# Optimization experiments

Hardware: AMD Instinct MI355X
Metric: run time of the kernel (lower is better)

## Reference

```python
import jax, jax.numpy as jnp
from jax import lax
import numpy as np

B, L, C, H, F = 8, 512, 512, 8, 2048
NC, NA, K, W, S = 4, 6, 5, 4, 50
HD = C // H
R = 2 * W + 1
PAD = (K - 1) // 2
H2 = 2
HD2 = C // H2
VOCAB = 256
EPS = 1e-6


def ln_ch(x, g, b):
    # LayerNorm over channel dim of (B,C,L) (torch transposes to (B,L,C), norms last dim)
    m = jnp.mean(x, axis=1, keepdims=True)
    v = jnp.mean((x - m) ** 2, axis=1, keepdims=True)
    return (x - m) * lax.rsqrt(v + EPS) * g[None, :, None] + b[None, :, None]


def conv1x1(w, b, x):
    # 1x1 Conv1d == channel-mixing matmul
    return jnp.einsum('oc,bcl->bol', w, x) + b[None, :, None]


def forward_fn(tokens, style_values, mask, embed,
               cw_dw_w, cw_dw_b, cw_ln_g, cw_ln_b, cw_pw1_w, cw_pw1_b,
               cw_pw2_w, cw_pw2_b, cw_gamma,
               aq_w, aq_b, ak_w, ak_b, av_w, av_b, ao_w, ao_b,
               rel_k_emb, rel_v_emb, ln1_g, ln1_b, ln2_g, ln2_b,
               ffn_w1, ffn_b1, ffn_w2, ffn_b2,
               style_key, sq_w, sq_b, sk_w, sk_b, sv_w, sv_b, so_w, so_b,
               sn_g, sn_b):
    x = embed[tokens]                 # (B,L,C)
    x = jnp.transpose(x, (0, 2, 1))   # (B,C,L)

    # --- ConvNeXt stack ---
    for i in range(NC):
        x = x * mask
        res = x
        xp = jnp.pad(x, ((0, 0), (0, 0), (PAD, PAD)), mode='edge')  # replicate pad
        h = lax.conv_general_dilated(xp, cw_dw_w[i][:, None, :], (1,), 'VALID',
                                     feature_group_count=C,
                                     dimension_numbers=('NCH', 'OIH', 'NCH'))
        h = h + cw_dw_b[i][None, :, None]
        h = h * mask
        h = ln_ch(h, cw_ln_g[i], cw_ln_b[i])
        h = conv1x1(cw_pw1_w[i], cw_pw1_b[i], h)
        h = jax.nn.gelu(h, approximate=False)
        h = conv1x1(cw_pw2_w[i], cw_pw2_b[i], h)
        x = res + cw_gamma[i][None, :, None] * h
        x = x * mask

    # --- AttnEncoder with windowed relative-position attention ---
    x = x * mask
    attn_mask = mask[:, :, :, None] * mask[:, :, None, :]   # (B,1,L,L)
    t = jnp.arange(L)
    diff = t[None, :] - t[:, None]
    wmask = (jnp.abs(diff) <= W).astype(x.dtype)             # (L,L)
    idx = jnp.clip(diff, -W, W) + W                          # (L,L) in [0,2W]
    scale = HD ** -0.5
    for i in range(NA):
        res = x
        q = conv1x1(aq_w[i], aq_b[i], x).reshape(B, H, HD, L).transpose(0, 1, 3, 2) * scale
        k = conv1x1(ak_w[i], ak_b[i], x).reshape(B, H, HD, L).transpose(0, 1, 3, 2)
        v = conv1x1(av_w[i], av_b[i], x).reshape(B, H, HD, L).transpose(0, 1, 3, 2)
        scores = jnp.einsum('bhld,bhmd->bhlm', q, k)
        rel_k = rel_k_emb[i][idx]                             # (L,L,HD)
        scores = scores + jnp.einsum('bhld,lmd->bhlm', q, rel_k) * wmask[None, None]
        scores = jnp.where(attn_mask == 0, -10000.0, scores)
        attn = jax.nn.softmax(scores, axis=-1)
        out = jnp.einsum('bhlm,bhmd->bhld', attn, v)
        rel_v = rel_v_emb[i][idx] * wmask[:, :, None]         # (L,L,HD)
        out = out + jnp.einsum('bhlm,lmd->bhld', attn, rel_v)
        out = out.transpose(0, 1, 3, 2).reshape(B, C, L)
        out = conv1x1(ao_w[i], ao_b[i], out)
        x = ln_ch(res + out, ln1_g[i], ln1_b[i])
        h = conv1x1(ffn_w1[i], ffn_b1[i], x * mask)
        h = jax.nn.relu(h) * mask
        h = conv1x1(ffn_w2[i], ffn_b2[i], h) * mask
        x = ln_ch(x + h, ln2_g[i], ln2_b[i])
    x = x * mask

    # --- StyleAttention ---
    xt = jnp.transpose(x, (0, 2, 1))          # (B,L,C)
    mask_t = jnp.transpose(mask, (0, 2, 1))   # (B,L,1)
    sscale = C ** -0.5                         # torch uses full dim, not head_dim

    def style_layer(xin, i):
        q = (xin @ sq_w[i].T + sq_b[i]).reshape(B, L, H2, HD2)
        kk = jnp.tanh(style_key[0] @ sk_w[i].T + sk_b[i]).reshape(S, H2, HD2)
        vals = jnp.broadcast_to(style_values, (B, S, C))
        vv = (vals @ sv_w[i].T + sv_b[i]).reshape(B, S, H2, HD2)
        sc = jnp.einsum('bthd,shd->hbts', q, kk) * sscale
        a = jax.nn.softmax(sc, axis=-1)
        a = jnp.where(mask_t[None] == 0, 0.0, a)
        o = jnp.einsum('hbts,bshd->bthd', a, vv).reshape(B, L, C)
        o = o @ so_w[i].T + so_b[i]
        return o * mask_t

    out1 = style_layer(xt, 0)
    x1 = xt + out1
    out2 = style_layer(x1, 1)
    x2 = xt + out2
    m = jnp.mean(x2, axis=-1, keepdims=True)
    var = jnp.mean((x2 - m) ** 2, axis=-1, keepdims=True)
    xn = (x2 - m) * lax.rsqrt(var + EPS) * sn_g + sn_b
    x = jnp.transpose(xn, (0, 2, 1)) * mask
    return x


def setup_inputs() -> dict:
    key = jax.random.key(0)
    kit = iter(jax.random.split(key, 48))

    def rn(shape, s=0.02):
        return jax.random.normal(next(kit), shape, jnp.float32) * s

    inp = {
        'tokens': jax.random.randint(next(kit), (B, L), 0, VOCAB),
        'style_values': rn((1, S, C), 1.0),
        'mask': jnp.ones((B, 1, L), jnp.float32),
        'embed': rn((VOCAB, C), 1.0),
        'cw_dw_w': rn((NC, C, K)), 'cw_dw_b': jnp.zeros((NC, C)),
        'cw_ln_g': jnp.ones((NC, C)), 'cw_ln_b': jnp.zeros((NC, C)),
        'cw_pw1_w': rn((NC, 4 * C, C)), 'cw_pw1_b': jnp.zeros((NC, 4 * C)),
        'cw_pw2_w': rn((NC, C, 4 * C)), 'cw_pw2_b': jnp.zeros((NC, C)),
        'cw_gamma': jnp.full((NC, C), 1e-6, jnp.float32),
        'aq_w': rn((NA, C, C)), 'aq_b': jnp.zeros((NA, C)),
        'ak_w': rn((NA, C, C)), 'ak_b': jnp.zeros((NA, C)),
        'av_w': rn((NA, C, C)), 'av_b': jnp.zeros((NA, C)),
        'ao_w': rn((NA, C, C)), 'ao_b': jnp.zeros((NA, C)),
        'rel_k_emb': rn((NA, R, HD)), 'rel_v_emb': rn((NA, R, HD)),
        'ln1_g': jnp.ones((NA, C)), 'ln1_b': jnp.zeros((NA, C)),
        'ln2_g': jnp.ones((NA, C)), 'ln2_b': jnp.zeros((NA, C)),
        'ffn_w1': rn((NA, F, C)), 'ffn_b1': jnp.zeros((NA, F)),
        'ffn_w2': rn((NA, C, F)), 'ffn_b2': jnp.zeros((NA, C)),
        'style_key': rn((1, S, C)),
        'sq_w': rn((2, C, C)), 'sq_b': jnp.zeros((2, C)),
        'sk_w': rn((2, C, C)), 'sk_b': jnp.zeros((2, C)),
        'sv_w': rn((2, C, C)), 'sv_b': jnp.zeros((2, C)),
        'so_w': rn((2, C, C)), 'so_b': jnp.zeros((2, C)),
        'sn_g': jnp.ones((C,)), 'sn_b': jnp.zeros((C,)),
    }
    return inp


def reference(tokens, style_values, mask, embed,
              cw_dw_w, cw_dw_b, cw_ln_g, cw_ln_b, cw_pw1_w, cw_pw1_b,
              cw_pw2_w, cw_pw2_b, cw_gamma,
              aq_w, aq_b, ak_w, ak_b, av_w, av_b, ao_w, ao_b,
              rel_k_emb, rel_v_emb, ln1_g, ln1_b, ln2_g, ln2_b,
              ffn_w1, ffn_b1, ffn_w2, ffn_b2,
              style_key, sq_w, sq_b, sk_w, sk_b, sv_w, sv_b, so_w, so_b,
              sn_g, sn_b):
    return forward_fn(tokens, style_values, mask, embed,
                      cw_dw_w, cw_dw_b, cw_ln_g, cw_ln_b, cw_pw1_w, cw_pw1_b,
                      cw_pw2_w, cw_pw2_b, cw_gamma,
                      aq_w, aq_b, ak_w, ak_b, av_w, av_b, ao_w, ao_b,
                      rel_k_emb, rel_v_emb, ln1_g, ln1_b, ln2_g, ln2_b,
                      ffn_w1, ffn_b1, ffn_w2, ffn_b2,
                      style_key, sq_w, sq_b, sk_w, sk_b, sv_w, sv_b, so_w, so_b,
                      sn_g, sn_b)
```

## Files before the change

kernel.cpp:

```cpp
#include <hip/hip_runtime.h>
#include <cstdint>

#define Bb 8
#define Ll 512
#define Cc 512
#define Hh 8
#define HD 64
#define Ff 2048
#define Ss 50
#define NROWS 4096
#define QKVS 1536

typedef __attribute__((ext_vector_type(8))) short short8v;
typedef __attribute__((ext_vector_type(4))) float f32x4;

__device__ __forceinline__ float wave_sum(float v){
  #pragma unroll
  for (int o=32;o>=1;o>>=1) v += __shfl_xor(v,o);
  return v;
}
__device__ __forceinline__ float wave_max(float v){
  #pragma unroll
  for (int o=32;o>=1;o>>=1) v = fmaxf(v,__shfl_xor(v,o));
  return v;
}
__device__ __forceinline__ float bf2f(unsigned short u){
  return __uint_as_float(((unsigned)u) << 16);
}

__device__ __forceinline__ void splitc(float a, unsigned short& hi, unsigned short& lo){
  unsigned u = __float_as_uint(a);
  hi = (unsigned short)(u >> 16);
  float l = a - __uint_as_float(u & 0xFFFF0000u);
  lo = (unsigned short)(__float_as_uint(l) >> 16);
}
__device__ __forceinline__ void split4(float4 v, unsigned short* hi, unsigned short* lo){
  unsigned short h0,h1,h2,h3,l0,l1,l2,l3;
  splitc(v.x,h0,l0); splitc(v.y,h1,l1); splitc(v.z,h2,l2); splitc(v.w,h3,l3);
  *(ushort4*)hi = make_ushort4(h0,h1,h2,h3);
  *(ushort4*)lo = make_ushort4(l0,l1,l2,l3);
}

__global__ __launch_bounds__(256) void split_all(
    const float* __restrict__ pw1w, const float* __restrict__ pw2w,
    const float* __restrict__ aow,  const float* __restrict__ f1w,
    const float* __restrict__ f2w,  const float* __restrict__ sqw,
    const float* __restrict__ sow,
    const float* __restrict__ aqw, const float* __restrict__ akw,
    const float* __restrict__ avw,
    unsigned short* __restrict__ pw1h, unsigned short* __restrict__ pw1l,
    unsigned short* __restrict__ pw2h, unsigned short* __restrict__ pw2l,
    unsigned short* __restrict__ aoh,  unsigned short* __restrict__ aol,
    unsigned short* __restrict__ f1h,  unsigned short* __restrict__ f1l,
    unsigned short* __restrict__ f2h,  unsigned short* __restrict__ f2l,
    unsigned short* __restrict__ sqh,  unsigned short* __restrict__ sql,
    unsigned short* __restrict__ soh,  unsigned short* __restrict__ sol,
    unsigned short* __restrict__ qkvh, unsigned short* __restrict__ qkvl)
{
  int seg = blockIdx.y;
  if (seg == 7){
    const int n4 = 6*QKVS*512/4;
    for (int i = blockIdx.x*256 + threadIdx.x; i < n4; i += gridDim.x*256){
      int e = i << 2;
      int layer = e / 786432;
      int r = e - layer*786432;
      int which = r >> 18;
      int off = r & 262143;
      const float* s = (which==0) ? aqw : (which==1) ? akw : avw;
      float4 vv = *(const float4*)(s + (size_t)layer*262144 + off);
      split4(vv, (unsigned short*)((ushort4*)qkvh + i),
                 (unsigned short*)((ushort4*)qkvl + i));
    }
    return;
  }
  const float* src; unsigned short* hi; unsigned short* lo; int n4;
  switch(seg){
    case 0: src=pw1w; hi=pw1h; lo=pw1l; n4=1048576; break;
    case 1: src=pw2w; hi=pw2h; lo=pw2l; n4=1048576; break;
    case 2: src=aow;  hi=aoh;  lo=aol;  n4=393216;  break;
    case 3: src=f1w;  hi=f1h;  lo=f1l;  n4=1572864; break;
    case 4: src=f2w;  hi=f2h;  lo=f2l;  n4=1572864; break;
    case 5: src=sqw;  hi=sqh;  lo=sql;  n4=131072;  break;
    default: src=sow; hi=soh;  lo=sol;  n4=131072;  break;
  }
  for (int i = blockIdx.x*256 + threadIdx.x; i < n4; i += gridDim.x*256){
    float4 v = ((const float4*)src)[i];
    split4(v, (unsigned short*)((ushort4*)hi + i), (unsigned short*)((ushort4*)lo + i));
  }
}

__global__ __launch_bounds__(128) void embed_k(const int* __restrict__ tok,
    const float* __restrict__ emb, const float* __restrict__ mask,
    float* __restrict__ x){
  int n = blockIdx.x;
  int t = tok[n];
  float m = mask[n];
  float4 v = ((const float4*)(emb + ((size_t)t<<9)))[threadIdx.x];
  v.x*=m; v.y*=m; v.z*=m; v.w*=m;
  ((float4*)(x + ((size_t)n<<9)))[threadIdx.x] = v;
}

__global__ __launch_bounds__(128) void dwln_k(const float* __restrict__ x,
    const float* __restrict__ w, const float* __restrict__ bias,
    const float* __restrict__ mask, const float* __restrict__ g,
    const float* __restrict__ bt, unsigned short* __restrict__ yh,
    unsigned short* __restrict__ yl){
  __shared__ float ws1[2], ws2[2];
  int n = blockIdx.x; int b_ = n >> 9, l = n & 511;
  int c0 = threadIdx.x * 4;
  float a0=bias[c0], a1=bias[c0+1], a2=bias[c0+2], a3=bias[c0+3];
  #pragma unroll
  for (int k=0;k<5;k++){
    int ls = l + k - 2; ls = ls < 0 ? 0 : (ls > 511 ? 511 : ls);
    const float4 xv = *(const float4*)&x[((size_t)(b_*512 + ls) << 9) + c0];
    a0 += w[(c0+0)*5+k]*xv.x;
    a1 += w[(c0+1)*5+k]*xv.y;
    a2 += w[(c0+2)*5+k]*xv.z;
    a3 += w[(c0+3)*5+k]*xv.w;
  }
  float mm = mask[n];
  a0*=mm; a1*=mm; a2*=mm; a3*=mm;
  int wv = threadIdx.x >> 6, ln_ = threadIdx.x & 63;
  float s = wave_sum(a0+a1+a2+a3);
  if (ln_ == 0) ws1[wv] = s;
  __syncthreads();
  float mean = (ws1[0] + ws1[1]) * (1.f/512.f);
  float d0=a0-mean, d1=a1-mean, d2=a2-mean, d3=a3-mean;
  float sq = wave_sum(d0*d0+d1*d1+d2*d2+d3*d3);
  if (ln_ == 0) ws2[wv] = sq;
  __syncthreads();
  float var = (ws2[0] + ws2[1]) * (1.f/512.f);
  float inv = 1.f/sqrtf(var + 1e-6f);
  float4 gv = *(const float4*)&g[c0];
  float4 bv = *(const float4*)&bt[c0];
  float4 o;
  o.x = d0*inv*gv.x + bv.x;
  o.y = d1*inv*gv.y + bv.y;
  o.z = d2*inv*gv.z + bv.z;
  o.w = d3*inv*gv.w + bv.w;
  size_t base = ((size_t)n << 9) + c0;
  split4(o, yh+base, yl+base);
}

template<bool SPLIT, bool MASK>
__global__ __launch_bounds__(256) void ln_rows(const float* __restrict__ x,
    const float* __restrict__ g, const float* __restrict__ bt,
    const float* __restrict__ rowmask,
    float* __restrict__ y, unsigned short* __restrict__ yh,
    unsigned short* __restrict__ yl, int nrows){
  int wid = threadIdx.x >> 6, lane = threadIdx.x & 63;
  int row = blockIdx.x*4 + wid;
  if (row >= nrows) return;
  const float4* xr = (const float4*)(x + ((size_t)row<<9));
  float4 a = xr[lane*2], b = xr[lane*2+1];
  float s = a.x+a.y+a.z+a.w+b.x+b.y+b.z+b.w;
  s = wave_sum(s);
  float m = s * (1.f/512.f);
  float d0=a.x-m,d1=a.y-m,d2=a.z-m,d3=a.w-m,d4=b.x-m,d5=b.y-m,d6=b.z-m,d7=b.w-m;
  float sq = d0*d0+d1*d1+d2*d2+d3*d3+d4*d4+d5*d5+d6*d6+d7*d7;
  sq = wave_sum(sq);
  float var = sq * (1.f/512.f);
  float inv = 1.f/sqrtf(var + 1e-6f);
  const float4* gr = (const float4*)g; const float4* br = (const float4*)bt;
  float4 g0=gr[lane*2], g1=gr[lane*2+1], b0=br[lane*2], b1=br[lane*2+1];
  float4 o0, o1;
  o0.x=d0*inv*g0.x+b0.x; o0.y=d1*inv*g0.y+b0.y; o0.z=d2*inv*g0.z+b0.z; o0.w=d3*inv*g0.w+b0.w;
  o1.x=d4*inv*g1.x+b1.x; o1.y=d5*inv*g1.y+b1.y; o1.z=d6*inv*g1.z+b1.z; o1.w=d7*inv*g1.w+b1.w;
  if constexpr (MASK){
    float mf = rowmask[row];
    o0.x*=mf; o0.y*=mf; o0.z*=mf; o0.w*=mf;
    o1.x*=mf; o1.y*=mf; o1.z*=mf; o1.w*=mf;
  }
  float4* yr = (float4*)(y + ((size_t)row<<9));
  yr[lane*2]=o0; yr[lane*2+1]=o1;
  if constexpr (SPLIT){
    size_t base = ((size_t)row<<9) + lane*8;
    split4(o0, yh+base,   yl+base);
    split4(o1, yh+base+4, yl+base+4);
  }
}

#define EPI_BIAS 0
#define EPI_SCALE 1
#define EPI_GELU 2
#define EPI_RES 3
#define EPI_RELU_MASK 4
#define EPI_RES_MASK 5
#define EPI_RES_GAMMA_MASK 6
#define EPI_TANH 7
#define EPI_QKV 8

__global__ __launch_bounds__(256) void style_prep(
    const float* __restrict__ style_key, const float* __restrict__ style_v,
    const float* __restrict__ sk_w, const float* __restrict__ sk_b,
    const float* __restrict__ sv_w, const float* __restrict__ sv_b,
    float* __restrict__ KK, float* __restrict__ VV)
{
  __shared__ float As[16][68];
  __shared__ float Bs[16][68];
  int sel = blockIdx.y;
  const float* A = (sel < 2) ? style_key : style_v;
  const float* W = (sel==0) ? sk_w : (sel==1) ? sk_w+262144 :
                   (sel==2) ? sv_w : sv_w+262144;
  const float* bias = (sel==0) ? sk_b : (sel==1) ? sk_b+512 :
                      (sel==2) ? sv_b : sv_b+512;
  float* Y = (sel==0) ? KK : (sel==1) ? KK+25600 :
             (sel==2) ? VV : VV+25600;
  bool do_tanh = (sel < 2);
  const int N = 50, K = 512, O = 512;
  int t = threadIdx.x;
  int tx = t & 15, ty = t >> 4;
  int col0 = blockIdx.x << 6;
  int lr = t >> 2, lk = (t & 3) << 2;
  float acc[4][4] = {};
  int ar = lr;
  bool arok = ar < N;
  const float* Ap = A + (size_t)(arok ? ar : 0) * K + lk;
  const float* Wp = W + (size_t)(col0 + lr) * K + lk;
  for (int k0 = 0; k0 < K; k0 += 16) {
    float4 av;
    if (arok) av = *(const float4*)(Ap + k0);
    else { av.x=0;av.y=0;av.z=0;av.w=0; }
    float4 bv = *(const float4*)(Wp + k0);
    As[lk+0][lr]=av.x; As[lk+1][lr]=av.y; As[lk+2][lr]=av.z; As[lk+3][lr]=av.w;
    Bs[lk+0][lr]=bv.x; Bs[lk+1][lr]=bv.y; Bs[lk+2][lr]=bv.z; Bs[lk+3][lr]=bv.w;
    __syncthreads();
    #pragma unroll
    for (int k=0;k<16;k++){
      float4 af = *(const float4*)&As[k][ty<<2];
      float4 bf = *(const float4*)&Bs[k][tx<<2];
      float a4[4]={af.x,af.y,af.z,af.w};
      float b4[4]={bf.x,bf.y,bf.z,bf.w};
      #pragma unroll
      for (int i=0;i<4;i++)
        #pragma unroll
        for (int j=0;j<4;j++)
          acc[i][j] += a4[i]*b4[j];
    }
    __syncthreads();
  }
  #pragma unroll
  for (int i=0;i<4;i++){
    int row = (ty<<2) + i;
    if (row >= N) break;
    int colb = col0 + (tx<<2);
    float vv_[4];
    #pragma unroll
    for (int j=0;j<4;j++){
      float v = acc[i][j] + bias[colb+j];
      if (do_tanh) v = tanhf(v);
      vv_[j]=v;
    }
    float4 ov; ov.x=vv_[0]; ov.y=vv_[1]; ov.z=vv_[2]; ov.w=vv_[3];
    *(float4*)(Y + (size_t)row*O + colb) = ov;
  }
}

template<int EPI, bool AMASK, int OUT, int NF>
__global__ __launch_bounds__(256) void gemm_ps(
    const unsigned short* __restrict__ Ah, const unsigned short* __restrict__ Al,
    const unsigned short* __restrict__ Wh, const unsigned short* __restrict__ Wl,
    const float* __restrict__ bias, const float* __restrict__ res,
    const float* __restrict__ gamma, const float* __restrict__ rowmask,
    float* __restrict__ Y, unsigned short* __restrict__ Yh,
    unsigned short* __restrict__ Yl, unsigned short* __restrict__ VTh,
    unsigned short* __restrict__ VTl, int K, int O, float scale)
{
  __shared__ unsigned short AhS[2][64][40], AlS[2][64][40];
  __shared__ unsigned short BhS[2][NF*32][40], BlS[2][NF*32][40];
  int t = threadIdx.x;
  int row0 = blockIdx.y << 6;
  int col0 = blockIdx.x << (NF==4 ? 7 : 6);
  int lane = t & 63, wid = t >> 6;
  int wr = wid >> 1, wc = wid & 1;

  int sr = t >> 2, sc = (t & 3) << 3;
  const unsigned short* Ahg = Ah + (size_t)(row0 + sr)*K + sc;
  const unsigned short* Alg = Al + (size_t)(row0 + sr)*K + sc;
  const unsigned short* Bhg = Wh + (size_t)(col0 + sr)*K + sc;
  const unsigned short* Blg = Wl + (size_t)(col0 + sr)*K + sc;
  float am = 1.f;
  if (AMASK) am = rowmask[row0 + sr];

  f32x4 acc[2][NF] = {};
  int nsteps = K >> 5;
  short8v ah_, al_, bh0_, bl0_, bh1_, bl1_;
  ah_ = *(const short8v*)(Ahg);
  al_ = *(const short8v*)(Alg);
  bh0_ = *(const short8v*)(Bhg);
  bl0_ = *(const short8v*)(Blg);
  if constexpr (NF==4){
    bh1_ = *(const short8v*)(Bhg + (size_t)64*K);
    bl1_ = *(const short8v*)(Blg + (size_t)64*K);
  }
  if (AMASK && am == 0.f){ ah_ ^= ah_; al_ ^= al_; }
  *(short8v*)&AhS[0][sr][sc] = ah_;
  *(short8v*)&AlS[0][sr][sc] = al_;
  *(short8v*)&BhS[0][sr][sc] = bh0_;
  *(short8v*)&BlS[0][sr][sc] = bl0_;
  if constexpr (NF==4){
    *(short8v*)&BhS[0][sr+64][sc] = bh1_;
    *(short8v*)&BlS[0][sr+64][sc] = bl1_;
  }

  int st = 0;
  for (int s = 0; s < nsteps; ++s){
    if (s+1 < nsteps){
      int ko = (s+1) << 5;
      ah_ = *(const short8v*)(Ahg + ko);
      al_ = *(const short8v*)(Alg + ko);
      bh0_ = *(const short8v*)(Bhg + ko);
      bl0_ = *(const short8v*)(Blg + ko);
      if constexpr (NF==4){
        bh1_ = *(const short8v*)(Bhg + (size_t)64*K + ko);
        bl1_ = *(const short8v*)(Blg + (size_t)64*K + ko);
      }
      if (AMASK && am == 0.f){ ah_ ^= ah_; al_ ^= al_; }
    }
    __syncthreads();
    int fr = lane & 15, fc = (lane >> 4) << 3;
    short8v ahf[2], alf[2], bhf[NF], blf[NF];
    #pragma unroll
    for (int mt=0; mt<2; ++mt){
      int r = (wr<<5) + (mt<<4) + fr;
      ahf[mt] = *(const short8v*)&AhS[st][r][fc];
      alf[mt] = *(const short8v*)&AlS[st][r][fc];
    }
    #pragma unroll
    for (int nt=0; nt<NF; ++nt){
      int r = (NF==4 ? (wc<<6) : (wc<<5)) + (nt<<4) + fr;
      bhf[nt] = *(const short8v*)&BhS[st][r][fc];
      blf[nt] = *(const short8v*)&BlS[st][r][fc];
    }
    #pragma unroll
    for (int mt=0; mt<2; ++mt)
      #pragma unroll
      for (int nt=0; nt<NF; ++nt){
        f32x4 c = acc[mt][nt];
        c = __builtin_amdgcn_mfma_f32_16x16x32_bf16(ahf[mt], bhf[nt], c, 0,0,0);
        c = __builtin_amdgcn_mfma_f32_16x16x32_bf16(ahf[mt], blf[nt], c, 0,0,0);
        c = __builtin_amdgcn_mfma_f32_16x16x32_bf16(alf[mt], bhf[nt], c, 0,0,0);
        acc[mt][nt] = c;
      }
    if (s+1 < nsteps){
      int nb = st ^ 1;
      *(short8v*)&AhS[nb][sr][sc] = ah_;
      *(short8v*)&AlS[nb][sr][sc] = al_;
      *(short8v*)&BhS[nb][sr][sc] = bh0_;
      *(short8v*)&BlS[nb][sr][sc] = bl0_;
      if constexpr (NF==4){
        *(short8v*)&BhS[nb][sr+64][sc] = bh1_;
        *(short8v*)&BlS[nb][sr+64][sc] = bl1_;
      }
    }
    st ^= 1;
  }

  int rb = row0 + (wr<<5) + ((lane>>4)<<2);
  int cb = col0 + (NF==4 ? (wc<<6) : (wc<<5)) + (lane & 15);
  float bs[NF], gm[NF];
  int which = 0;
  if constexpr (EPI==EPI_QKV) which = blockIdx.x >> 2;
  #pragma unroll
  for (int nt=0; nt<NF; ++nt){
    int col = cb + (nt<<4);
    if constexpr (EPI==EPI_QKV){
      const float* bp = (which==0) ? bias : (which==1) ? res : gamma;
      bs[nt] = bp[col & 511];
    } else {
      bs[nt] = bias[col];
      if constexpr (EPI==EPI_RES_GAMMA_MASK) gm[nt] = gamma[col];
    }
  }
  float qscale = 1.f;
  if constexpr (EPI==EPI_QKV) qscale = (which==0) ? scale : 1.f;

  if constexpr (OUT==2){
    if (which == 2){
      #pragma unroll
      for (int mt=0; mt<2; ++mt){
        int row = rb + (mt<<4);
        int b = row >> 9, tok = row & 511;
        #pragma unroll
        for (int nt=0; nt<NF; ++nt){
          int dglob = cb + (nt<<4) - 1024;
          size_t vt = ((size_t)b*512 + dglob)*512 + tok;
          unsigned short h4[4], l4[4];
          #pragma unroll
          for (int j=0; j<4; ++j)
            splitc(acc[mt][nt][j] + bs[nt], h4[j], l4[j]);
          *(ushort4*)&VTh[vt] = make_ushort4(h4[0],h4[1],h4[2],h4[3]);
          *(ushort4*)&VTl[vt] = make_ushort4(l4[0],l4[1],l4[2],l4[3]);
        }
      }
      return;
    }
    #pragma unroll
    for (int mt=0; mt<2; ++mt)
      #pragma unroll
      for (int j=0; j<4; ++j){
        int row = rb + (mt<<4) + j;
        #pragma unroll
        for (int nt=0; nt<NF; ++nt){
          float v = (acc[mt][nt][j] + bs[nt]) * qscale;
          size_t oidx = (size_t)row*O + cb + (nt<<4);
          unsigned short h,l; splitc(v,h,l); Yh[oidx]=h; Yl[oidx]=l;
        }
      }
// ... 241 lines not shown
  short8v ah0 = *(const short8v*)&Qh[fr][fc];
  short8v ah1 = *(const short8v*)&Qh[fr][32+fc];
  short8v al0 = *(const short8v*)&Ql[fr][fc];
  short8v al1 = *(const short8v*)&Ql[fr][32+fc];

  if (w == 0){
    short8v rh0 = *(const short8v*)&Rkh[fr][fc];
    short8v rh1 = *(const short8v*)&Rkh[fr][32+fc];
    short8v rl0 = *(const short8v*)&Rkl[fr][fc];
    short8v rl1 = *(const short8v*)&Rkl[fr][32+fc];
    f32x4 c4 = {};
    c4 = __builtin_amdgcn_mfma_f32_16x16x32_bf16(ah0,rh0,c4,0,0,0);
    c4 = __builtin_amdgcn_mfma_f32_16x16x32_bf16(ah1,rh1,c4,0,0,0);
    c4 = __builtin_amdgcn_mfma_f32_16x16x32_bf16(ah0,rl0,c4,0,0,0);
    c4 = __builtin_amdgcn_mfma_f32_16x16x32_bf16(ah1,rl1,c4,0,0,0);
    c4 = __builtin_amdgcn_mfma_f32_16x16x32_bf16(al0,rh0,c4,0,0,0);
    c4 = __builtin_amdgcn_mfma_f32_16x16x32_bf16(al1,rh1,c4,0,0,0);
    #pragma unroll
    for (int j = 0; j < 4; ++j) qrel[qbase + j][fr] = c4[j];
  }
  __syncthreads();

  f32x4 sreg[8];
  #pragma unroll
  for (int tt = 0; tt < 8; ++tt){
    int br = tt*64 + w*16 + fr;
    const unsigned short* krh = Ph_g + (rowoff + br)*QKVS + 512 + h*64;
    const unsigned short* krl = Pl_g + (rowoff + br)*QKVS + 512 + h*64;
    short8v bh0 = *(const short8v*)(krh + fc);
    short8v bh1 = *(const short8v*)(krh + 32 + fc);
    short8v bl0 = *(const short8v*)(krl + fc);
    short8v bl1 = *(const short8v*)(krl + 32 + fc);
    f32x4 c4 = {};
    c4 = __builtin_amdgcn_mfma_f32_16x16x32_bf16(ah0,bh0,c4,0,0,0);
    c4 = __builtin_amdgcn_mfma_f32_16x16x32_bf16(ah1,bh1,c4,0,0,0);
    c4 = __builtin_amdgcn_mfma_f32_16x16x32_bf16(ah0,bl0,c4,0,0,0);
    c4 = __builtin_amdgcn_mfma_f32_16x16x32_bf16(ah1,bl1,c4,0,0,0);
    c4 = __builtin_amdgcn_mfma_f32_16x16x32_bf16(al0,bh0,c4,0,0,0);
    c4 = __builtin_amdgcn_mfma_f32_16x16x32_bf16(al1,bh1,c4,0,0,0);
    int m = tt*64 + w*16 + fr;
    float mm_ = ms_[m];
    #pragma unroll
    for (int j = 0; j < 4; ++j){
      int q = qbase + j;
      int l = l0 + q;
      float s = c4[j];
      int dlt = m - l + 4;
      if (dlt >= 0 && dlt <= 8) s += qrel[q][dlt];
      if (ms_[l] * mm_ == 0.f) s = -10000.f;
      c4[j] = s;
    }
    sreg[tt] = c4;
  }

  float mx[4], sm[4], inv[4];
  #pragma unroll
  for (int j = 0; j < 4; ++j){
    float v = sreg[0][j];
    #pragma unroll
    for (int tt = 1; tt < 8; ++tt) v = fmaxf(v, sreg[tt][j]);
    #pragma unroll
    for (int o = 8; o >= 1; o >>= 1) v = fmaxf(v, __shfl_xor(v, o));
    mx[j] = v;
  }
  if (fr == 0){
    #pragma unroll
    for (int j = 0; j < 4; ++j) red1[w][qbase + j] = mx[j];
  }
  __syncthreads();
  #pragma unroll
  for (int j = 0; j < 4; ++j){
    int q = qbase + j;
    mx[j] = fmaxf(fmaxf(red1[0][q], red1[1][q]), fmaxf(red1[2][q], red1[3][q]));
  }
  #pragma unroll
  for (int j = 0; j < 4; ++j) sm[j] = 0.f;
  #pragma unroll
  for (int tt = 0; tt < 8; ++tt){
    f32x4 c4 = sreg[tt];
    #pragma unroll
    for (int j = 0; j < 4; ++j){
      float e = expf(c4[j] - mx[j]);
      c4[j] = e;
      sm[j] += e;
    }
    sreg[tt] = c4;
  }
  #pragma unroll
  for (int j = 0; j < 4; ++j){
    float v = sm[j];
    #pragma unroll
    for (int o = 8; o >= 1; o >>= 1) v += __shfl_xor(v, o);
    sm[j] = v;
  }
  if (fr == 0){
    #pragma unroll
    for (int j = 0; j < 4; ++j) red2[w][qbase + j] = sm[j];
  }
  #pragma unroll
  for (int tt = 0; tt < 8; ++tt){
    int m = tt*64 + w*16 + fr;
    #pragma unroll
    for (int j = 0; j < 4; ++j){
      unsigned short hh, ll_;
      splitc(sreg[tt][j], hh, ll_);
      Sh[qbase + j][m] = hh; Sl[qbase + j][m] = ll_;
    }
  }
  __syncthreads();
  #pragma unroll
  for (int j = 0; j < 4; ++j){
    int q = qbase + j;
    inv[j] = 1.f / (red2[0][q] + red2[1][q] + red2[2][q] + red2[3][q]);
  }

  f32x4 oacc = {};
  const unsigned short* vrh = VTh_g + ((size_t)b_*512 + h*64 + w*16 + fr)*512;
  const unsigned short* vrl = VTl_g + ((size_t)b_*512 + h*64 + w*16 + fr)*512;
  #pragma unroll
  for (int tt = 0; tt < 8; ++tt){
    #pragma unroll
    for (int ks = 0; ks < 2; ++ks){
      int moff = tt*64 + ks*32 + fc;
      short8v ah = *(const short8v*)&Sh[fr][moff];
      short8v al = *(const short8v*)&Sl[fr][moff];
      short8v bh = *(const short8v*)(vrh + moff);
      short8v bl = *(const short8v*)(vrl + moff);
      oacc = __builtin_amdgcn_mfma_f32_16x16x32_bf16(ah,bh,oacc,0,0,0);
      oacc = __builtin_amdgcn_mfma_f32_16x16x32_bf16(ah,bl,oacc,0,0,0);
      oacc = __builtin_amdgcn_mfma_f32_16x16x32_bf16(al,bh,oacc,0,0,0);
    }
  }
  {
    int d = w*16 + fr;
    #pragma unroll
    for (int j = 0; j < 4; ++j){
      int q = qbase + j;
      int l = l0 + q;
      float val = oacc[j];
      #pragma unroll
      for (int dlt = 0; dlt < 9; ++dlt){
        int m = l + dlt - 4;
        if (m >= 0 && m < 512){
          float e = bf2f(Sh[q][m]) + bf2f(Sl[q][m]);
          val += e * rv[dlt][d];
        }
      }
      val *= inv[j];
      unsigned short hh, ll_; splitc(val, hh, ll_);
      size_t oidx = ((rowoff + l) << 9) + h*64 + d;
      Oh[oidx] = hh; Ol[oidx] = ll_;
    }
  }
}

__global__ __launch_bounds__(128) void style_attn_k(const float* __restrict__ Q,
    const float* __restrict__ kk, const float* __restrict__ vv,
    const float* __restrict__ mask, unsigned short* __restrict__ Oh,
    unsigned short* __restrict__ Ol){
  int n = blockIdx.x;
  int h = threadIdx.x >> 6, lane = threadIdx.x & 63;
  __shared__ float qh[512];
  __shared__ float aw[2][64];
  {
    float4 v = ((const float4*)(Q + ((size_t)n<<9)))[threadIdx.x];
    *(float4*)&qh[threadIdx.x*4] = v;
  }
  __syncthreads();
  float sc;
  if (lane < 50){
    float s = 0.f;
    const float* kr = kk + lane*512 + h*256;
    const float* qr = qh + h*256;
    for (int d4 = 0; d4 < 64; ++d4){
      float4 kv = *(const float4*)&kr[d4*4];
      s += qr[d4*4]*kv.x + qr[d4*4+1]*kv.y + qr[d4*4+2]*kv.z + qr[d4*4+3]*kv.w;
    }
    sc = s * 0.044194173824159216f;
  } else sc = -1e30f;
  float mx = wave_max(sc);
  float ex = (lane < 50) ? expf(sc - mx) : 0.f;
  float sm = wave_sum(ex);
  float keep = (mask[n] == 0.f) ? 0.f : 1.f;
  aw[h][lane] = ex / sm * keep;
  __syncthreads();
  float4 acc; acc.x=0; acc.y=0; acc.z=0; acc.w=0;
  const float* vb = vv + h*256 + lane*4;
  for (int s = 0; s < 50; ++s){
    float a = aw[h][s];
    const float4 vvv = *(const float4*)&vb[(size_t)s*512];
    acc.x += a*vvv.x; acc.y += a*vvv.y; acc.z += a*vvv.z; acc.w += a*vvv.w;
  }
  size_t oidx = ((size_t)n<<9) + h*256 + lane*4;
  split4(acc, Oh+oidx, Ol+oidx);
}

__global__ __launch_bounds__(256) void transpose_out_k(const float* __restrict__ xn,
    const float* __restrict__ mask, float* __restrict__ out){
  __shared__ float tile[32][33];
  int b_ = blockIdx.z; int c0 = blockIdx.x*32; int l0 = blockIdx.y*32;
  int tx = threadIdx.x & 31, ty = threadIdx.x >> 5;
  #pragma unroll
  for (int r=0;r<4;r++){
    int l = l0 + ty + r*8;
    tile[ty + r*8][tx] = xn[(((size_t)(b_*512 + l))<<9) + c0 + tx];
  }
  __syncthreads();
  float mm = mask[b_*512 + l0 + tx];
  #pragma unroll
  for (int r=0;r<4;r++){
    int c = c0 + ty + r*8;
    out[(((size_t)(b_*512 + c))<<9) + l0 + tx] = tile[tx][ty + r*8] * mm;
  }
}

extern "C" void kernel_launch(void* const* d_in, const int* in_sizes, int n_in,
                              void* d_out, int out_size, void* d_ws, size_t ws_size,
                              hipStream_t stream) {
  const int*   tokens   = (const int*)  d_in[0];
  const float* style_v  = (const float*)d_in[1];
  const float* mask     = (const float*)d_in[2];
  const float* embed_w  = (const float*)d_in[3];
  const float* cw_dw_w  = (const float*)d_in[4];
  const float* cw_dw_b  = (const float*)d_in[5];
  const float* cw_ln_g  = (const float*)d_in[6];
  const float* cw_ln_b  = (const float*)d_in[7];
  const float* cw_pw1_w = (const float*)d_in[8];
  const float* cw_pw1_b = (const float*)d_in[9];
  const float* cw_pw2_w = (const float*)d_in[10];
  const float* cw_pw2_b = (const float*)d_in[11];
  const float* cw_gamma = (const float*)d_in[12];
  const float* aq_w = (const float*)d_in[13];
  const float* aq_b = (const float*)d_in[14];
  const float* ak_w = (const float*)d_in[15];
  const float* ak_b = (const float*)d_in[16];
  const float* av_w = (const float*)d_in[17];
  const float* av_b = (const float*)d_in[18];
  const float* ao_w = (const float*)d_in[19];
  const float* ao_b = (const float*)d_in[20];
  const float* rel_k = (const float*)d_in[21];
  const float* rel_v = (const float*)d_in[22];
  const float* ln1_g = (const float*)d_in[23];
  const float* ln1_b = (const float*)d_in[24];
  const float* ln2_g = (const float*)d_in[25];
  const float* ln2_b = (const float*)d_in[26];
  const float* ffn_w1 = (const float*)d_in[27];
  const float* ffn_b1 = (const float*)d_in[28];
  const float* ffn_w2 = (const float*)d_in[29];
  const float* ffn_b2 = (const float*)d_in[30];
  const float* style_key = (const float*)d_in[31];
  const float* sq_w = (const float*)d_in[32];
  const float* sq_b = (const float*)d_in[33];
  const float* sk_w = (const float*)d_in[34];
  const float* sk_b = (const float*)d_in[35];
  const float* sv_w = (const float*)d_in[36];
  const float* sv_b = (const float*)d_in[37];
  const float* so_w = (const float*)d_in[38];
  const float* so_b = (const float*)d_in[39];
  const float* sn_g = (const float*)d_in[40];
  const float* sn_b = (const float*)d_in[41];

  const int N = NROWS;
  char* cur = (char*)d_ws;
  auto nextF = [&](size_t n)->float*{ float* p=(float*)cur; cur += n*sizeof(float); return p; };
  auto nextU = [&](size_t n)->unsigned short*{ unsigned short* p=(unsigned short*)cur; cur += n*2; return p; };

  float* X   = nextF((size_t)N*512);
  float* T   = nextF((size_t)N*512);
  float* Qb  = nextF((size_t)N*512);
  float* Vb  = nextF((size_t)N*512);
  float* KK  = nextF(2*50*512);
  float* VV  = nextF(2*50*512);
  unsigned short* Xh = nextU((size_t)N*512);
  unsigned short* Xl = nextU((size_t)N*512);
  unsigned short* Th = nextU((size_t)N*512);
  unsigned short* Tl = nextU((size_t)N*512);
  unsigned short* Hbh = nextU((size_t)N*2048);
  unsigned short* Hbl = nextU((size_t)N*2048);
  unsigned short* QKVh = nextU((size_t)N*QKVS);
  unsigned short* QKVl = nextU((size_t)N*QKVS);
  unsigned short* VTh = nextU((size_t)8*512*512);
  unsigned short* VTl = nextU((size_t)8*512*512);
  unsigned short* pw1h = nextU(4194304); unsigned short* pw1l = nextU(4194304);
  unsigned short* pw2h = nextU(4194304); unsigned short* pw2l = nextU(4194304);
  unsigned short* qkvh = nextU((size_t)6*QKVS*512); unsigned short* qkvl = nextU((size_t)6*QKVS*512);
  unsigned short* aoh  = nextU(1572864); unsigned short* aol  = nextU(1572864);
  unsigned short* f1h  = nextU(6291456); unsigned short* f1l  = nextU(6291456);
  unsigned short* f2h  = nextU(6291456); unsigned short* f2l  = nextU(6291456);
  unsigned short* sqh  = nextU(524288);  unsigned short* sql  = nextU(524288);
  unsigned short* soh  = nextU(524288);  unsigned short* sol  = nextU(524288);

  split_all<<<dim3(512,8),256,0,stream>>>(cw_pw1_w, cw_pw2_w, ao_w, ffn_w1,
      ffn_w2, sq_w, so_w, aq_w, ak_w, av_w,
      pw1h, pw1l, pw2h, pw2l, aoh, aol, f1h, f1l, f2h, f2l,
      sqh, sql, soh, sol, qkvh, qkvl);

  dim3 gm512(8,64), gbig2048(16,32), gbigqkv(12,32);

  embed_k<<<4096,128,0,stream>>>(tokens, embed_w, mask, X);

  for (int i=0;i<4;i++){
    dwln_k<<<4096,128,0,stream>>>(X, cw_dw_w + (size_t)i*512*5, cw_dw_b + i*512,
        mask, cw_ln_g+i*512, cw_ln_b+i*512, Th, Tl);
    gemm_big<EPI_GELU,false,1><<<gbig2048,256,0,stream>>>(Th, Tl,
        pw1h + (size_t)i*1048576, pw1l + (size_t)i*1048576,
        cw_pw1_b+i*2048, nullptr, nullptr, nullptr, nullptr, Hbh, Hbl,
        nullptr, nullptr, 512, 2048, 0.f);
    if (i < 3)
      gemm_ps<EPI_RES_GAMMA_MASK,false,0,2><<<gm512,256,0,stream>>>(Hbh, Hbl,
          pw2h + (size_t)i*1048576, pw2l + (size_t)i*1048576,
          cw_pw2_b+i*512, X, cw_gamma+i*512, mask, X, nullptr, nullptr,
          nullptr, nullptr, 2048, 512, 0.f);
    else
      gemm_ps<EPI_RES_GAMMA_MASK,false,3,2><<<gm512,256,0,stream>>>(Hbh, Hbl,
          pw2h + (size_t)i*1048576, pw2l + (size_t)i*1048576,
          cw_pw2_b+i*512, X, cw_gamma+i*512, mask, X, Xh, Xl,
          nullptr, nullptr, 2048, 512, 0.f);
  }

  for (int i=0;i<6;i++){
    gemm_big<EPI_QKV,false,2><<<gbigqkv,256,0,stream>>>(Xh, Xl,
        qkvh + (size_t)i*QKVS*512, qkvl + (size_t)i*QKVS*512,
        aq_b+i*512, ak_b+i*512, av_b+i*512, nullptr, nullptr, QKVh, QKVl,
        VTh, VTl, 512, QKVS, 0.125f);
    attn_mf<<<2048,256,0,stream>>>(QKVh, QKVl, VTh, VTl,
        rel_k + (size_t)i*9*64, rel_v + (size_t)i*9*64, mask, Th, Tl);
    gemm_ps<EPI_RES,false,0,2><<<gm512,256,0,stream>>>(Th, Tl,
        aoh + (size_t)i*262144, aol + (size_t)i*262144,
        ao_b+i*512, X, nullptr, nullptr, Qb, nullptr, nullptr,
        nullptr, nullptr, 512, 512, 0.f);
    ln_rows<true,false><<<1024,256,0,stream>>>(Qb, ln1_g+i*512, ln1_b+i*512,
        nullptr, X, Xh, Xl, N);
    gemm_big<EPI_RELU_MASK,true,1><<<gbig2048,256,0,stream>>>(Xh, Xl,
        f1h + (size_t)i*1048576, f1l + (size_t)i*1048576,
        ffn_b1+i*2048, nullptr, nullptr, mask, nullptr, Hbh, Hbl,
        nullptr, nullptr, 512, 2048, 0.f);
    gemm_ps<EPI_RES_MASK,false,0,2><<<gm512,256,0,stream>>>(Hbh, Hbl,
        f2h + (size_t)i*1048576, f2l + (size_t)i*1048576,
        ffn_b2+i*512, X, nullptr, mask, Qb, nullptr, nullptr,
        nullptr, nullptr, 2048, 512, 0.f);
    if (i < 5)
      ln_rows<true,false><<<1024,256,0,stream>>>(Qb, ln2_g+i*512, ln2_b+i*512,
          nullptr, X, Xh, Xl, N);
    else
      ln_rows<true,true><<<1024,256,0,stream>>>(Qb, ln2_g+i*512, ln2_b+i*512,
          mask, X, Xh, Xl, N);
  }

  style_prep<<<dim3(8,4),256,0,stream>>>(style_key, style_v, sk_w, sk_b,
      sv_w, sv_b, KK, VV);

  gemm_ps<EPI_BIAS,false,0,2><<<gm512,256,0,stream>>>(Xh, Xl, sqh, sql,
      sq_b, nullptr, nullptr, nullptr, Qb, nullptr, nullptr,
      nullptr, nullptr, 512, 512, 0.f);
  style_attn_k<<<4096,128,0,stream>>>(Qb, KK, VV, mask, Th, Tl);
  gemm_ps<EPI_RES_MASK,false,1,2><<<gm512,256,0,stream>>>(Th, Tl, soh, sol,
      so_b, X, nullptr, mask, nullptr, Hbh, Hbl,
      nullptr, nullptr, 512, 512, 0.f);
  gemm_ps<EPI_BIAS,false,0,2><<<gm512,256,0,stream>>>(Hbh, Hbl, sqh+262144, sql+262144,
      sq_b+512, nullptr, nullptr, nullptr, Qb, nullptr, nullptr,
      nullptr, nullptr, 512, 512, 0.f);
  style_attn_k<<<4096,128,0,stream>>>(Qb, KK+25600, VV+25600, mask, Th, Tl);
  gemm_ps<EPI_RES_MASK,false,0,2><<<gm512,256,0,stream>>>(Th, Tl, soh+262144, sol+262144,
      so_b+512, X, nullptr, mask, Vb, nullptr, nullptr,
      nullptr, nullptr, 512, 512, 0.f);

  ln_rows<false,false><<<1024,256,0,stream>>>(Vb, sn_g, sn_b, nullptr,
      Qb, nullptr, nullptr, N);
  transpose_out_k<<<dim3(16,16,8),256,0,stream>>>(Qb, mask, (float*)d_out);
}
```

Measured before the change: 1.890 ms.

## Run style attention on MFMA with split-bf16 Q, K and transposed V

Replaces the scalar FP32 style-attention kernel, which used one block per query row, with an MFMA kernel. Each block handles 16 rows for both heads and uses split hi/lo bf16 operands (three MFMAs per product) for Q·K and P·V. style_prep now writes K and a transposed V in split bf16 with padding to 64 keys, and the Q projection emits split bf16 instead of fp32. This moves the style attention onto the matrix units at the cost of serial softmax on 32 threads and a small loss in precision from the split-bf16 scheme.

```diff
diff --git a/kernel.cpp b/kernel.cpp
--- a/kernel.cpp
+++ b/kernel.cpp
@@ -17,11 +17,6 @@
 __device__ __forceinline__ float wave_sum(float v){
   #pragma unroll
   for (int o=32;o>=1;o>>=1) v += __shfl_xor(v,o);
-  return v;
-}
-__device__ __forceinline__ float wave_max(float v){
-  #pragma unroll
-  for (int o=32;o>=1;o>>=1) v = fmaxf(v,__shfl_xor(v,o));
   return v;
 }
 __device__ __forceinline__ float bf2f(unsigned short u){
@@ -194,28 +189,27 @@
     const float* __restrict__ style_key, const float* __restrict__ style_v,
     const float* __restrict__ sk_w, const float* __restrict__ sk_b,
     const float* __restrict__ sv_w, const float* __restrict__ sv_b,
-    float* __restrict__ KK, float* __restrict__ VV)
+    unsigned short* __restrict__ KKh, unsigned short* __restrict__ KKl,
+    unsigned short* __restrict__ VTh_s, unsigned short* __restrict__ VTl_s)
 {
   __shared__ float As[16][68];
   __shared__ float Bs[16][68];
   int sel = blockIdx.y;
-  const float* A = (sel < 2) ? style_key : style_v;
+  bool is_k = (sel < 2);
+  int layer = sel & 1;
+  const float* A = is_k ? style_key : style_v;
   const float* W = (sel==0) ? sk_w : (sel==1) ? sk_w+262144 :
                    (sel==2) ? sv_w : sv_w+262144;
   const float* bias = (sel==0) ? sk_b : (sel==1) ? sk_b+512 :
                       (sel==2) ? sv_b : sv_b+512;
-  float* Y = (sel==0) ? KK : (sel==1) ? KK+25600 :
-             (sel==2) ? VV : VV+25600;
-  bool do_tanh = (sel < 2);
-  const int N = 50, K = 512, O = 512;
+  const int N = 50, K = 512;
   int t = threadIdx.x;
   int tx = t & 15, ty = t >> 4;
   int col0 = blockIdx.x << 6;
   int lr = t >> 2, lk = (t & 3) << 2;
   float acc[4][4] = {};
-  int ar = lr;
-  bool arok = ar < N;
-  const float* Ap = A + (size_t)(arok ? ar : 0) * K + lk;
+  bool arok = lr < N;
+  const float* Ap = A + (size_t)(arok ? lr : 0) * K + lk;
   const float* Wp = W + (size_t)(col0 + lr) * K + lk;
   for (int k0 = 0; k0 < K; k0 += 16) {
     float4 av;
@@ -242,18 +236,114 @@
   #pragma unroll
   for (int i=0;i<4;i++){
     int row = (ty<<2) + i;
-    if (row >= N) break;
-    int colb = col0 + (tx<<2);
-    float vv_[4];
     #pragma unroll
     for (int j=0;j<4;j++){
-      float v = acc[i][j] + bias[colb+j];
-      if (do_tanh) v = tanhf(v);
-      vv_[j]=v;
-    }
-    float4 ov; ov.x=vv_[0]; ov.y=vv_[1]; ov.z=vv_[2]; ov.w=vv_[3];
-    *(float4*)(Y + (size_t)row*O + colb) = ov;
-  }
+      int col = col0 + (tx<<2) + j;
+      int head = col >> 8, d = col & 255;
+      float v = 0.f;
+      if (row < N){
+        v = acc[i][j] + bias[col];
+        if (is_k) v = tanhf(v);
+      }
+      unsigned short hh, ll_;
+      splitc(v, hh, ll_);
+      if (is_k){
+        size_t o = (((size_t)layer*2 + head)<<14) + row*256 + d;
+        KKh[o]=hh; KKl[o]=ll_;
+      } else {
+        size_t o = (((size_t)layer*2 + head)<<14) + d*64 + row;
+        VTh_s[o]=hh; VTl_s[o]=ll_;
+      }
+    }
+  }
+}
+
+__global__ __launch_bounds__(256) void style_mf(
+    const unsigned short* __restrict__ Qh_g, const unsigned short* __restrict__ Ql_g,
+    const unsigned short* __restrict__ KKh, const unsigned short* __restrict__ KKl,
+    const unsigned short* __restrict__ VTh_s, const unsigned short* __restrict__ VTl_s,
+    const float* __restrict__ mask,
+    unsigned short* __restrict__ Oh, unsigned short* __restrict__ Ol)
+{
+  __shared__ float Sc[2][16][68];
+  __shared__ unsigned short Pph[2][16][72], Ppl[2][16][72];
+  int t = threadIdx.x, lane = t & 63, w = t >> 6;
+  int head = w >> 1, nh = w & 1;
+  int rowbase = blockIdx.x * 16;
+  int fr = lane & 15, fc = (lane >> 4) << 3, qbase = (lane >> 4) << 2;
+
+  f32x4 s2[2] = {};
+  #pragma unroll
+  for (int ks = 0; ks < 8; ++ks){
+    size_t qoff = (size_t)(rowbase + fr)*512 + head*256 + ks*32 + fc;
+    short8v ah = *(const short8v*)(Qh_g + qoff);
+    short8v al = *(const short8v*)(Ql_g + qoff);
+    #pragma unroll
+    for (int nt = 0; nt < 2; ++nt){
+      int key = nh*32 + nt*16 + fr;
+      size_t ko = (((size_t)head)<<14) + key*256 + ks*32 + fc;
+      short8v bh = *(const short8v*)(KKh + ko);
+      short8v bl = *(const short8v*)(KKl + ko);
+      f32x4 c = s2[nt];
+      c = __builtin_amdgcn_mfma_f32_16x16x32_bf16(ah,bh,c,0,0,0);
+      c = __builtin_amdgcn_mfma_f32_16x16x32_bf16(ah,bl,c,0,0,0);
+      c = __builtin_amdgcn_mfma_f32_16x16x32_bf16(al,bh,c,0,0,0);
+      s2[nt] = c;
+    }
+  }
+  #pragma unroll
+  for (int nt = 0; nt < 2; ++nt)
+    #pragma unroll
+    for (int j = 0; j < 4; ++j)
+      Sc[head][qbase+j][nh*32 + nt*16 + fr] = s2[nt][j] * 0.044194173824159216f;
+  __syncthreads();
+
+  if (t < 32){
+    int h2 = t >> 4, r = t & 15;
+    float mx = -3.4e38f;
+    for (int ss = 0; ss < 50; ++ss) mx = fmaxf(mx, Sc[h2][r][ss]);
+    float sum = 0.f;
+    for (int ss = 0; ss < 50; ++ss) sum += expf(Sc[h2][r][ss] - mx);
+    float keep = (mask[rowbase + r] == 0.f) ? 0.f : 1.f;
+    float inv = keep / sum;
+    for (int ss = 0; ss < 64; ++ss){
+      float p = (ss < 50) ? expf(Sc[h2][r][ss] - mx) * inv : 0.f;
+      unsigned short hh, ll_;
+      splitc(p, hh, ll_);
+      Pph[h2][r][ss] = hh; Ppl[h2][r][ss] = ll_;
+    }
+  }
+  __syncthreads();
+
+  f32x4 av[8] = {};
+  #pragma unroll
+  for (int ks = 0; ks < 2; ++ks){
+    short8v ah = *(const short8v*)&Pph[head][fr][ks*32 + fc];
+    short8v al = *(const short8v*)&Ppl[head][fr][ks*32 + fc];
+    #pragma unroll
+    for (int nt = 0; nt < 8; ++nt){
+      int d = nh*128 + nt*16 + fr;
+      size_t vo = (((size_t)head)<<14) + d*64 + ks*32 + fc;
+      short8v bh = *(const short8v*)(VTh_s + vo);
+      short8v bl = *(const short8v*)(VTl_s + vo);
+      f32x4 c = av[nt];
+      c = __builtin_amdgcn_mfma_f32_16x16x32_bf16(ah,bh,c,0,0,0);
+      c = __builtin_amdgcn_mfma_f32_16x16x32_bf16(ah,bl,c,0,0,0);
+      c = __builtin_amdgcn_mfma_f32_16x16x32_bf16(al,bh,c,0,0,0);
+      av[nt] = c;
+    }
+  }
+  #pragma unroll
+  for (int nt = 0; nt < 8; ++nt)
+    #pragma unroll
+    for (int j = 0; j < 4; ++j){
+      int row = rowbase + qbase + j;
+      int d = nh*128 + nt*16 + fr;
+      unsigned short hh, ll_;
+      splitc(av[nt][j], hh, ll_);
+      size_t o = (size_t)row*512 + head*256 + d;
+      Oh[o] = hh; Ol[o] = ll_;
+    }
 }
 
 template<int EPI, bool AMASK, int OUT, int NF>
@@ -801,47 +891,6 @@
       Oh[oidx] = hh; Ol[oidx] = ll_;
     }
   }
-}
-
-__global__ __launch_bounds__(128) void style_attn_k(const float* __restrict__ Q,
-    const float* __restrict__ kk, const float* __restrict__ vv,
-    const float* __restrict__ mask, unsigned short* __restrict__ Oh,
-    unsigned short* __restrict__ Ol){
-  int n = blockIdx.x;
-  int h = threadIdx.x >> 6, lane = threadIdx.x & 63;
-  __shared__ float qh[512];
-  __shared__ float aw[2][64];
-  {
-    float4 v = ((const float4*)(Q + ((size_t)n<<9)))[threadIdx.x];
-    *(float4*)&qh[threadIdx.x*4] = v;
-  }
-  __syncthreads();
-  float sc;
-  if (lane < 50){
-    float s = 0.f;
-    const float* kr = kk + lane*512 + h*256;
-    const float* qr = qh + h*256;
-    for (int d4 = 0; d4 < 64; ++d4){
-      float4 kv = *(const float4*)&kr[d4*4];
-      s += qr[d4*4]*kv.x + qr[d4*4+1]*kv.y + qr[d4*4+2]*kv.z + qr[d4*4+3]*kv.w;
-    }
-    sc = s * 0.044194173824159216f;
-  } else sc = -1e30f;
-  float mx = wave_max(sc);
-  float ex = (lane < 50) ? expf(sc - mx) : 0.f;
-  float sm = wave_sum(ex);
-  float keep = (mask[n] == 0.f) ? 0.f : 1.f;
-  aw[h][lane] = ex / sm * keep;
-  __syncthreads();
-  float4 acc; acc.x=0; acc.y=0; acc.z=0; acc.w=0;
-  const float* vb = vv + h*256 + lane*4;
-  for (int s = 0; s < 50; ++s){
-    float a = aw[h][s];
-    const float4 vvv = *(const float4*)&vb[(size_t)s*512];
-    acc.x += a*vvv.x; acc.y += a*vvv.y; acc.z += a*vvv.z; acc.w += a*vvv.w;
-  }
-  size_t oidx = ((size_t)n<<9) + h*256 + lane*4;
-  split4(acc, Oh+oidx, Ol+oidx);
 }
 
 __global__ __launch_bounds__(256) void transpose_out_k(const float* __restrict__ xn,
@@ -918,8 +967,6 @@
   float* T   = nextF((size_t)N*512);
   float* Qb  = nextF((size_t)N*512);
   float* Vb  = nextF((size_t)N*512);
-  float* KK  = nextF(2*50*512);
-  float* VV  = nextF(2*50*512);
   unsigned short* Xh = nextU((size_t)N*512);
   unsigned short* Xl = nextU((size_t)N*512);
   unsigned short* Th = nextU((size_t)N*512);
@@ -938,6 +985,8 @@
   unsigned short* f2h  = nextU(6291456); unsigned short* f2l  = nextU(6291456);
   unsigned short* sqh  = nextU(524288);  unsigned short* sql  = nextU(524288);
   unsigned short* soh  = nextU(524288);  unsigned short* sol  = nextU(524288);
+  unsigned short* KKsh = nextU(65536); unsigned short* KKsl = nextU(65536);
+  unsigned short* VTsh = nextU(65536); unsigned short* VTsl = nextU(65536);
 
   split_all<<<dim3(512,8),256,0,stream>>>(cw_pw1_w, cw_pw2_w, ao_w, ffn_w1,
       ffn_w2, sq_w, so_w, aq_w, ak_w, av_w,
@@ -997,19 +1046,21 @@
   }
 
   style_prep<<<dim3(8,4),256,0,stream>>>(style_key, style_v, sk_w, sk_b,
-      sv_w, sv_b, KK, VV);
-
-  gemm_ps<EPI_BIAS,false,0,2><<<gm512,256,0,stream>>>(Xh, Xl, sqh, sql,
-      sq_b, nullptr, nullptr, nullptr, Qb, nullptr, nullptr,
+      sv_w, sv_b, KKsh, KKsl, VTsh, VTsl);
+
+  gemm_ps<EPI_BIAS,false,1,2><<<gm512,256,0,stream>>>(Xh, Xl, sqh, sql,
+      sq_b, nullptr, nullptr, nullptr, nullptr, QKVh, QKVl,
       nullptr, nullptr, 512, 512, 0.f);
-  style_attn_k<<<4096,128,0,stream>>>(Qb, KK, VV, mask, Th, Tl);
+  style_mf<<<256,256,0,stream>>>(QKVh, QKVl, KKsh, KKsl, VTsh, VTsl,
+      mask, Th, Tl);
   gemm_ps<EPI_RES_MASK,false,1,2><<<gm512,256,0,stream>>>(Th, Tl, soh, sol,
       so_b, X, nullptr, mask, nullptr, Hbh, Hbl,
       nullptr, nullptr, 512, 512, 0.f);
-  gemm_ps<EPI_BIAS,false,0,2><<<gm512,256,0,stream>>>(Hbh, Hbl, sqh+262144, sql+262144,
-      sq_b+512, nullptr, nullptr, nullptr, Qb, nullptr, nullptr,
+  gemm_ps<EPI_BIAS,false,1,2><<<gm512,256,0,stream>>>(Hbh, Hbl, sqh+262144, sql+262144,
+      sq_b+512, nullptr, nullptr, nullptr, nullptr, QKVh, QKVl,
       nullptr, nullptr, 512, 512, 0.f);
-  style_attn_k<<<4096,128,0,stream>>>(Qb, KK+25600, VV+25600, mask, Th, Tl);
+  style_mf<<<256,256,0,stream>>>(QKVh, QKVl, KKsh+32768, KKsl+32768,
+      VTsh+32768, VTsl+32768, mask, Th, Tl);
   gemm_ps<EPI_RES_MASK,false,0,2><<<gm512,256,0,stream>>>(Th, Tl, soh+262144, sol+262144,
       so_b+512, X, nullptr, mask, Vb, nullptr, nullptr,
       nullptr, nullptr, 512, 512, 0.f);
```

Result: faster. 1.804 ms (median of 2 runs) (-4.6%).
